# Performance work log

Measured on AMD Instinct MI355X. Metric: run time of the kernel, lower is better.

## Reference

```python
import jax, jax.numpy as jnp
import numpy as np
import math

B, S, H, NH = 8, 512, 1024, 16
DH = H // NH
MAX_REL = 64
LN_EPS = 1e-12


def _relpos_table(length, depth, max_rel=MAX_REL):
    # sinusoidal table over relative-distance vocab, gathered into [L, L, depth]
    vocab = 2 * max_rel + 1
    pos = np.arange(vocab, dtype=np.float32)[:, None]
    div = np.exp(np.arange(0, depth, 2, dtype=np.float32) * (-math.log(10000.0) / depth))
    table = np.zeros((vocab, depth), dtype=np.float32)
    table[:, 0::2] = np.sin(pos * div)
    table[:, 1::2] = np.cos(pos * div)
    r = np.arange(length)
    dist = np.clip(r[None, :] - r[:, None], -max_rel, max_rel) + max_rel  # [L,L], entry (i,j)=j-i
    return jnp.asarray(table[dist])  # [L, L, depth]


def _linear(x, W, b):  # torch layout: W [out, in]
    return jnp.einsum('...i,oi->...o', x, W) + b


def _gather_shift(seq, shift, valid_len):
    # seq [B,S,H]; out[i, j] = seq[i, j+shift[i]] for j < valid_len[i], else 0
    pos = jnp.arange(S)
    idx = jnp.clip(pos[None, :] + shift[:, None], 0, S - 1)  # [B,S]
    g = jnp.take_along_axis(seq, idx[:, :, None], axis=1)
    mask = pos[None, :] < valid_len[:, None]
    return jnp.where(mask[:, :, None], g, jnp.zeros((), seq.dtype))


def _nezha_attention(hs, enc, R, Wq, bq, Wk, bk, Wv, bv):
    def heads(x):  # [B,S,H] -> [B,NH,S,DH]
        return x.reshape(B, S, NH, DH).transpose(0, 2, 1, 3)
    q = heads(_linear(hs, Wq, bq))
    k = heads(_linear(enc, Wk, bk))
    v = heads(_linear(enc, Wv, bv))
    scores = jnp.einsum('bhqd,bhkd->bhqk', q, k)
    scores = scores + jnp.einsum('bhqd,qkd->bhqk', q, R)  # relative-key bias
    scores = scores / math.sqrt(DH)
    probs = jax.nn.softmax(scores, axis=-1)  # dropout: eval mode (identity)
    ctx = jnp.einsum('bhqk,bhkd->bhqd', probs, v)
    ctx = ctx + jnp.einsum('bhqk,qkd->bhqd', probs, R)  # relative-value term
    return ctx.transpose(0, 2, 1, 3).reshape(B, S, H)


def setup_inputs() -> dict:
    key = jax.random.key(0)
    ks = jax.random.split(key, 16)
    w = lambda k, shp: jax.random.normal(k, shp, jnp.float32) * 0.02
    return {
        'sequence_output': jax.random.normal(ks[0], (B, S, H), jnp.float32),
        'doc_len': jax.random.randint(ks[1], (B,), 0, 300, jnp.int32),
        'ques_len': jax.random.randint(ks[2], (B,), 0, 100, jnp.int32),
        'option_len': jax.random.randint(ks[3], (B,), 0, 100, jnp.int32),
        'Wq': w(ks[4], (H, H)), 'bq': jnp.zeros((H,), jnp.float32),
        'Wk': w(ks[5], (H, H)), 'bk': jnp.zeros((H,), jnp.float32),
        'Wv': w(ks[6], (H, H)), 'bv': jnp.zeros((H,), jnp.float32),
        'Wp': w(ks[7], (H, H)), 'bp': jnp.zeros((H,), jnp.float32),
        'Wo': w(ks[8], (H, H)), 'bo': jnp.zeros((H,), jnp.float32),
        'ln_g': jnp.ones((H,), jnp.float32), 'ln_b': jnp.zeros((H,), jnp.float32),
    }


def reference(sequence_output, doc_len, ques_len, option_len,
              Wq, bq, Wk, bk, Wv, bv, Wp, bp, Wo, bo, ln_g, ln_b):
    one = jnp.ones_like(doc_len)
    # seperate_seq (only the two tensors DUMA consumes)
    doc_seq = _gather_shift(sequence_output, one, doc_len)
    ques_opt = _gather_shift(sequence_output, doc_len + 1, ques_len + option_len)

    R = _relpos_table(S, DH)
    doc_enc = _nezha_attention(doc_seq, ques_opt, R, Wq, bq, Wk, bk, Wv, bv)
    qo_enc = _nezha_attention(ques_opt, doc_seq, R, Wq, bq, Wk, bk, Wv, bv)

    pooler = lambda x: jnp.tanh(_linear(x, Wp, bp))
    doc_pooled = pooler(doc_enc)
    qo_pooled = pooler(qo_enc)

    # BertSelfOutput: dense + (dropout=eval) + LayerNorm(residual)
    y = _linear(doc_pooled, Wo, bo) + qo_pooled
    mu = jnp.mean(y, axis=-1, keepdims=True)
    var = jnp.mean(jnp.square(y - mu), axis=-1, keepdims=True)
    y = (y - mu) * jax.lax.rsqrt(var + LN_EPS) * ln_g + ln_b

    return pooler(y)
```

## Files before the change

### kernel.cpp

```cpp
#include <hip/hip_runtime.h>
#include <hip/hip_bf16.h>
#include <cstdint>
#include <cstddef>

using bf16 = __hip_bfloat16;
typedef __attribute__((ext_vector_type(8))) short short8;
typedef __attribute__((ext_vector_type(4))) short short4v;
typedef __attribute__((ext_vector_type(4))) float f32x4;

#define KQLD 2048
#define SCL   0.18033688f
#define EXP2F(x) __builtin_amdgcn_exp2f(x)

__device__ __forceinline__ void gl2lds16(const bf16* g, void* l) {
  __builtin_amdgcn_global_load_lds((const __attribute__((address_space(1))) void*)g,
                                   (__attribute__((address_space(3))) void*)l, 16, 0, 0);
}

template<int ACT, bool OUTBF, bool HASB, int VTM>
__global__ __launch_bounds__(512)
void gemm_big(const bf16* __restrict__ A, const bf16* __restrict__ Bm,
              void* __restrict__ Cv, const float* __restrict__ bias,
              int N, int K, int lda, int ldb, int ldc, bf16* __restrict__ Vt)
{
  __shared__ __align__(16) short lA[3 * 4096];
  __shared__ __align__(16) short lB[3 * 8192];
  const int tid = threadIdx.x;
  int bx = blockIdx.x, by = blockIdx.y;
  {
    const int nwg = gridDim.x * gridDim.y;
    if ((nwg & 7) == 0) {
      int n = by * gridDim.x + bx;
      n = (n & 7) * (nwg >> 3) + (n >> 3);
      bx = n / gridDim.y;
      by = n % gridDim.y;
    }
  }
  const int m0 = bx * 128;
  const int n0 = by * 256;
  const int w = tid >> 6, lane = tid & 63;
  const int wr = (w >> 2) * 64, wc = (w & 3) * 64;
  const int lr = lane & 15, lg = lane >> 4;
  f32x4 acc[4][4] = {};
  const int ra = tid >> 2;
  const int xc = ((tid & 3) ^ ((tid >> 2) & 3)) * 8;
  const int e1 = tid + 512;
  const int rb1 = e1 >> 2;
  const bf16* pa0 = A + (long)(m0 + ra) * lda + xc;
  const bf16* pb0 = Bm + (long)(n0 + ra) * ldb + xc;
  const bf16* pb1 = Bm + (long)(n0 + rb1) * ldb + xc;

  #define GSTG(k0_, ofa_, ofb_) do {                  \
    gl2lds16(pa0 + (k0_), &lA[(ofa_) + tid * 8]);     \
    gl2lds16(pb0 + (k0_), &lB[(ofb_) + tid * 8]);     \
    gl2lds16(pb1 + (k0_), &lB[(ofb_) + e1 * 8]);      \
  } while (0)

  const int nT = K >> 5;
  GSTG(0, 0, 0);
  if (nT > 1) GSTG(32, 4096, 8192);
  if (nT > 2) asm volatile("s_waitcnt vmcnt(3)" ::: "memory");
  else        asm volatile("s_waitcnt vmcnt(0)" ::: "memory");
  __builtin_amdgcn_s_barrier();
  __builtin_amdgcn_sched_barrier(0);

  const int lgx = (lg ^ (lr & 3)) * 8;
  int oa = 0, oa1 = 4096, oa2 = 8192;
  int ob = 0, ob1 = 8192, ob2 = 16384;
  for (int t = 0; t < nT; ++t) {
    if (t + 2 < nT) GSTG((t + 2) * 32, oa2, ob2);
    short8 af[4], bfr[4];
    #pragma unroll
    for (int i = 0; i < 4; ++i) {
      af[i]  = *(const short8*)(&lA[oa + (wr + i * 16 + lr) * 32 + lgx]);
      bfr[i] = *(const short8*)(&lB[ob + (wc + i * 16 + lr) * 32 + lgx]);
    }
    #pragma unroll
    for (int mf = 0; mf < 4; ++mf)
      #pragma unroll
      for (int nf = 0; nf < 4; ++nf)
        acc[mf][nf] = __builtin_amdgcn_mfma_f32_16x16x32_bf16(af[mf], bfr[nf], acc[mf][nf], 0, 0, 0);
    if (t + 1 < nT) {
      if (t + 2 < nT) asm volatile("s_waitcnt vmcnt(3)" ::: "memory");
      else            asm volatile("s_waitcnt vmcnt(0)" ::: "memory");
      __builtin_amdgcn_s_barrier();
      __builtin_amdgcn_sched_barrier(0);
      int tmp = oa; oa = oa1; oa1 = oa2; oa2 = tmp;
      tmp = ob; ob = ob1; ob1 = ob2; ob2 = tmp;
    }
  }
  #undef GSTG

  #pragma unroll
  for (int nf = 0; nf < 4; ++nf) {
    const int col = n0 + wc + nf * 16 + lr;
    if (col >= N) continue;
    const float bv = HASB ? bias[col] : 0.0f;
    if (VTM && col >= 2048) {
      const int hd = col - 2048;
      const int d = hd & 63, hh = hd >> 6;
      #pragma unroll
      for (int mf = 0; mf < 4; ++mf) {
        const int row0 = m0 + wr + mf * 16 + lg * 4;
        const int zz = ((1 - (row0 >> 12)) << 7) | (((row0 >> 9) & 7) << 4) | hh;
        short4v pk;
        #pragma unroll
        for (int j = 0; j < 4; ++j)
          pk[j] = (short)__builtin_bit_cast(unsigned short,
                    __float2bfloat16(acc[mf][nf][j] + bv));
        *(short4v*)(Vt + ((long)(zz * 64 + d)) * 512 + (row0 & 511)) = pk;
      }
    } else {
      #pragma unroll
      for (int mf = 0; mf < 4; ++mf) {
        #pragma unroll
        for (int j = 0; j < 4; ++j) {
          const int row = m0 + wr + mf * 16 + lg * 4 + j;
          float x = acc[mf][nf][j] + bv;
          if (ACT == 1) x = tanhf(x);
          const long off = (long)row * ldc + col;
          if (OUTBF) ((bf16*)Cv)[off] = __float2bfloat16(x);
          else       ((float*)Cv)[off] = x;
        }
      }
    }
  }
}

template<int ACT, bool OUTBF, bool HASB>
__global__ __launch_bounds__(256)
void gemm_sm(const bf16* __restrict__ A, const bf16* __restrict__ Bm,
             void* __restrict__ Cv, const float* __restrict__ bias,
             int N, int K, int lda, int ldb, int ldc)
{
  __shared__ __align__(16) short lA[3 * 4096];
  __shared__ __align__(16) short lB[3 * 4096];
  const int tid = threadIdx.x;
  int bx = blockIdx.x, by = blockIdx.y;
  {
    const int nwg = gridDim.x * gridDim.y;
    if ((nwg & 7) == 0) {
      int n = by * gridDim.x + bx;
      n = (n & 7) * (nwg >> 3) + (n >> 3);
      bx = n / gridDim.y;
      by = n % gridDim.y;
    }
  }
  const int m0 = bx * 128;
  const int n0 = by * 128;
  const int w = tid >> 6, lane = tid & 63;
  const int wr = (w >> 1) * 64, wc = (w & 1) * 64;
  const int lr = lane & 15, lg = lane >> 4;
  f32x4 acc[4][4] = {};
  const int e0 = tid, e1 = tid + 256;
  const int r0_ = e0 >> 2;
  const int r1_ = e1 >> 2;
  const int xc = ((tid & 3) ^ ((tid >> 2) & 3)) * 8;
  const bf16* pa0 = A + (long)(m0 + r0_) * lda + xc;
  const bf16* pa1 = A + (long)(m0 + r1_) * lda + xc;
  const bf16* pb0 = Bm + (long)(n0 + r0_) * ldb + xc;
  const bf16* pb1 = Bm + (long)(n0 + r1_) * ldb + xc;

  #define GSTG2(k0_, off_) do {                       \
    gl2lds16(pa0 + (k0_), &lA[(off_) + e0 * 8]);      \
    gl2lds16(pa1 + (k0_), &lA[(off_) + e1 * 8]);      \
    gl2lds16(pb0 + (k0_), &lB[(off_) + e0 * 8]);      \
    gl2lds16(pb1 + (k0_), &lB[(off_) + e1 * 8]);      \
  } while (0)

  const int nT = K >> 5;
  GSTG2(0, 0);
  if (nT > 1) GSTG2(32, 4096);
  if (nT > 2) asm volatile("s_waitcnt vmcnt(4)" ::: "memory");
  else        asm volatile("s_waitcnt vmcnt(0)" ::: "memory");
  __builtin_amdgcn_s_barrier();
  __builtin_amdgcn_sched_barrier(0);

  const int lgx = (lg ^ (lr & 3)) * 8;
  int ofc = 0, of1 = 4096, of2 = 8192;
  for (int t = 0; t < nT; ++t) {
    if (t + 2 < nT) GSTG2((t + 2) * 32, of2);
    short8 af[4], bfr[4];
    #pragma unroll
    for (int i = 0; i < 4; ++i) {
      af[i]  = *(const short8*)(&lA[ofc + (wr + i * 16 + lr) * 32 + lgx]);
      bfr[i] = *(const short8*)(&lB[ofc + (wc + i * 16 + lr) * 32 + lgx]);
    }
    #pragma unroll
    for (int mf = 0; mf < 4; ++mf)
      #pragma unroll
      for (int nf = 0; nf < 4; ++nf)
        acc[mf][nf] = __builtin_amdgcn_mfma_f32_16x16x32_bf16(af[mf], bfr[nf], acc[mf][nf], 0, 0, 0);
    if (t + 1 < nT) {
      if (t + 2 < nT) asm volatile("s_waitcnt vmcnt(4)" ::: "memory");
      else            asm volatile("s_waitcnt vmcnt(0)" ::: "memory");
      __builtin_amdgcn_s_barrier();
      __builtin_amdgcn_sched_barrier(0);
      const int tmp = ofc; ofc = of1; of1 = of2; of2 = tmp;
    }
  }
  #undef GSTG2

  #pragma unroll
  for (int nf = 0; nf < 4; ++nf) {
    const int col = n0 + wc + nf * 16 + lr;
    if (col >= N) continue;
    const float bv = HASB ? bias[col] : 0.0f;
    #pragma unroll
    for (int mf = 0; mf < 4; ++mf) {
      #pragma unroll
      for (int j = 0; j < 4; ++j) {
        const int row = m0 + wr + mf * 16 + lg * 4 + j;
        float x = acc[mf][nf][j] + bv;
        if (ACT == 1) x = tanhf(x);
        const long off = (long)row * ldc + col;
        if (OUTBF) ((bf16*)Cv)[off] = __float2bfloat16(x);
        else       ((float*)Cv)[off] = x;
      }
    }
  }
}

__global__ __launch_bounds__(256)
void k_prep(const float* __restrict__ w0, const float* __restrict__ w1,
            const float* __restrict__ w2, const float* __restrict__ w3,
            const float* __restrict__ w4, bf16* __restrict__ wdst,
            const float* __restrict__ seq, const int* __restrict__ dl,
            const int* __restrict__ ql, const int* __restrict__ ol,
            bf16* __restrict__ X, bf16* __restrict__ tbl, bf16* __restrict__ tbt,
            const float* __restrict__ bq, const float* __restrict__ bk,
            const float* __restrict__ bv, float* __restrict__ biasq)
{
  const int bid = blockIdx.x, tid = threadIdx.x;
  if (bid < 5120) {
    const int bsel = bid >> 10;
    const float* s = bsel == 0 ? w0 : bsel == 1 ? w1 : bsel == 2 ? w2 : bsel == 3 ? w3 : w4;
    const float sc = (bsel == 0) ? SCL : 1.0f;
    const long loc = ((long)(bid & 1023) * 256 + tid) * 4;
    float4 v = *(const float4*)(s + loc);
    short4v pk;
    pk[0] = (short)__builtin_bit_cast(unsigned short, __float2bfloat16(v.x * sc));
    pk[1] = (short)__builtin_bit_cast(unsigned short, __float2bfloat16(v.y * sc));
    pk[2] = (short)__builtin_bit_cast(unsigned short, __float2bfloat16(v.z * sc));
    pk[3] = (short)__builtin_bit_cast(unsigned short, __float2bfloat16(v.w * sc));
    *(short4v*)(wdst + (long)bsel * 1048576 + loc) = pk;
  } else if (bid < 13312) {
    const int row = bid - 5120;
    const int c = tid * 4;
    const int b = (row >> 9) & 7, j = row & 511;
    int vlen, src;
    if (row < 4096) { vlen = dl[b]; src = (j + 1 > 511) ? 511 : j + 1; }
    else {
      vlen = ql[b] + ol[b];
      int s2 = j + dl[b] + 1;
      src = s2 > 511 ? 511 : (s2 < 0 ? 0 : s2);
    }
    float4 v = make_float4(0, 0, 0, 0);
    if (j < vlen) v = *(const float4*)(seq + ((long)b * 512 + src) * 1024 + c);
    short4v pk;
    pk[0] = (short)__builtin_bit_cast(unsigned short, __float2bfloat16(v.x));
    pk[1] = (short)__builtin_bit_cast(unsigned short, __float2bfloat16(v.y));
    pk[2] = (short)__builtin_bit_cast(unsigned short, __float2bfloat16(v.z));
    pk[3] = (short)__builtin_bit_cast(unsigned short, __float2bfloat16(v.w));
    *(short4v*)(X + (long)row * 1024 + c) = pk;
  } else {
    for (int idx = tid; idx < 144 * 64; idx += 256) {
      const int r = idx >> 6, d = idx & 63;
      float v = 0.0f;
      if (r < 129) {
        const float dv = powf(10000.0f, -(float)(d >> 1) / 32.0f);
        const float a = (float)r * dv;
        v = (d & 1) ? cosf(a) : sinf(a);
      }
      tbl[idx] = __float2bfloat16(v);
    }
    for (int idx = tid; idx < 64 * 160; idx += 256) {
      const int d = idx / 160, rr = idx % 160;
      float v = 0.0f;
      if (rr < 129) {
        const float dv = powf(10000.0f, -(float)(d >> 1) / 32.0f);
        const float a = (float)rr * dv;
        v = (d & 1) ? cosf(a) : sinf(a);
      }
      tbt[idx] = __float2bfloat16(v);
    }
    for (int idx = tid; idx < 3072; idx += 256) {
      float v = (idx < 1024) ? bq[idx] * SCL : (idx < 2048) ? bk[idx - 1024] : bv[idx - 2048];
      biasq[idx] = v;
    }
  }
}

__global__ __launch_bounds__(1024, 4)
void k_attn(const bf16* __restrict__ QKV, const bf16* __restrict__ Vt,
            const bf16* __restrict__ tbl, const bf16* __restrict__ tbt,
            bf16* __restrict__ ctx)
{
  __shared__ __align__(16) unsigned short s_kv[16384];
  __shared__ __align__(16) unsigned short s_ptile[16][16 * 72];
  __shared__ __align__(16) unsigned short s_m[16][16 * 132];

  const int tid = threadIdx.x;
  const int wv = tid >> 6, lane = tid & 63;
  const int lr = lane & 15, lg = lane >> 4;
  const int bid = blockIdx.x;
  const int xcd = bid & 7;
  const int idx = bid >> 3;
  const int z = (xcd << 5) | (idx >> 1);
  const int g = idx & 1;
  const int attn = z >> 7, b = (z >> 4) & 7, h = z & 15;
  const int qtok0 = attn * 4096 + b * 512;
  const int ktok0 = (1 - attn) * 4096 + b * 512;
  const int q0 = g * 256 + wv * 16;
  const int q = q0 + lr;

  unsigned short* ptile = s_ptile[wv];
  unsigned short* mrow  = s_m[wv];

  const bf16* Kbase = QKV + (long)ktok0 * KQLD + 1024 + h * 64;
  const bf16* Vbase = Vt + (long)z * (64 * 512);

  const int sl = tid & 511;
  const int rs = sl >> 3, cs = (sl & 7) * 8;
  const int scz = cs ^ ((rs & 7) << 3);
  const bool isV = tid >= 512;

  short8 qf[2];
  #pragma unroll
  for (int hh = 0; hh < 2; ++hh)
    qf[hh] = *(const short8*)(QKV + (long)(qtok0 + q0 + lr) * KQLD + h * 64 + hh * 32 + lg * 8);

  #define STAGE(kvb_, koff_, voff_) do {                                            \
    if (!isV) gl2lds16(Kbase + (long)((kvb_) + rs) * KQLD + scz, &s_kv[(koff_) + sl * 8]); \
    else      gl2lds16(Vbase + (long)rs * 512 + (kvb_) + scz,    &s_kv[(voff_) + sl * 8]); \
  } while (0)

  STAGE(0, 0, 8192);

  #pragma unroll
  for (int rt = 0; rt < 9; ++rt) {
    f32x4 qa = {};
    #pragma unroll
    for (int hh = 0; hh < 2; ++hh) {
      short8 ta = *(const short8*)(tbl + (rt * 16 + lr) * 64 + hh * 32 + lg * 8);
      qa = __builtin_amdgcn_mfma_f32_16x16x32_bf16(ta, qf[hh], qa, 0, 0, 0);
    }
    if (rt < 8 || lg == 0) {
      short4v pk;
      #pragma unroll
      for (int j = 0; j < 4; ++j)
        pk[j] = (short)__builtin_bit_cast(unsigned short, __float2bfloat16(qa[j]));
      *(short4v*)(&mrow[lr * 132 + rt * 16 + lg * 4]) = pk;
    }
  }

  const int hx = (lr >> 2) & 1;
  const int lgx8 = (lg ^ (lr & 3)) * 8;
  const int lrx64 = lr * 64;

  const float bias_lo = __bfloat162float(((const bf16*)mrow)[lr * 132 + 0]);
  const float bias_hi = __bfloat162float(((const bf16*)mrow)[lr * 132 + 128]);

  float l_run = 0.f, b0 = 0.f, b1 = 0.f;
  f32x4 cacc[4] = {};

  __syncthreads();

  #pragma unroll 2
  for (int t = 0; t < 8; ++t) {
    const int kvb = t * 64;
    const int koff = (t & 1) * 4096;
    const int voff = 8192 + koff;
    if (t < 7) { const int nk = ((t + 1) & 1) * 4096; STAGE(kvb + 64, nk, 8192 + nk); }

    f32x4 sc[4] = {};
    __builtin_amdgcn_s_setprio(1);
    #pragma unroll
    for (int hh = 0; hh < 2; ++hh) {
      const int cb = ((hh ^ hx) << 5) + lgx8;
      #pragma unroll
      for (int kb4 = 0; kb4 < 4; ++kb4) {
        short8 ak = *(const short8*)(&s_kv[koff + kb4 * 1024 + lrx64 + cb]);
        sc[kb4] = __builtin_amdgcn_mfma_f32_16x16x32_bf16(ak, qf[hh], sc[kb4], 0, 0, 0);
      }
    }
    __builtin_amdgcn_s_setprio(0);

    const int cls = (kvb + 63 <= q0 - 64) ? 0 : ((kvb >= q0 + 79) ? 2 : 1);

    float pacc[4];
    if (cls == 1) {
      const bool eLo = (kvb <= q0 - 49);
      const bool eHi = (kvb + 63 >= q0 + 64);
      short4v pks[4];
      #pragma unroll
      for (int kb4 = 0; kb4 < 4; ++kb4) {
        short4v pk;
        float ps = 0.f;
        #pragma unroll
        for (int j = 0; j < 4; ++j) {
          int rel = kvb + kb4 * 16 + 4 * lg + j - q;
          int rc = rel < -64 ? -64 : (rel > 64 ? 64 : rel);
          float bias = __bfloat162float(((const bf16*)mrow)[lr * 132 + rc + 64]);
          float p = EXP2F(sc[kb4][j] + bias);
          ps += p;
          if (eLo && rel <= -64) b0 += p;
          if (eHi && rel >= 64)  b1 += p;
          pk[j] = (short)__builtin_bit_cast(unsigned short, __float2bfloat16(p));
        }
        pks[kb4] = pk;
        pacc[kb4] = ps;
        *(short4v*)(&ptile[lr * 72 + kb4 * 16 + 4 * lg]) = pk;
      }
      l_run += (pacc[0] + pacc[1]) + (pacc[2] + pacc[3]);
      #pragma unroll
      for (int kb4 = 0; kb4 < 4; ++kb4)
        #pragma unroll
        for (int j = 0; j < 4; ++j) {
          int rel = kvb + kb4 * 16 + 4 * lg + j - q;
          if (rel > -64 && rel < 64)
            mrow[lr * 132 + rel + 63] = (unsigned short)pks[kb4][j];
        }
    } else {
      const float bc = (cls == 0) ? bias_lo : bias_hi;
      #pragma unroll
      for (int kb4 = 0; kb4 < 4; ++kb4) {
        short4v pk;
        float ps = 0.f;
        #pragma unroll
        for (int j = 0; j < 4; ++j) {
          float p = EXP2F(sc[kb4][j] + bc);
          ps += p;
          pk[j] = (short)__builtin_bit_cast(unsigned short, __float2bfloat16(p));
        }
        pacc[kb4] = ps;
        *(short4v*)(&ptile[lr * 72 + kb4 * 16 + 4 * lg]) = pk;
      }
      const float ts = (pacc[0] + pacc[1]) + (pacc[2] + pacc[3]);
      l_run += ts;
      if (cls == 0) b0 += ts; else b1 += ts;
    }

    __builtin_amdgcn_s_setprio(1);
    #pragma unroll
    for (int c2 = 0; c2 < 2; ++c2) {
      short8 pa = *(const short8*)(&ptile[lr * 72 + c2 * 32 + lg * 8]);
      const int cb = ((c2 ^ hx) << 5) + lgx8;
      #pragma unroll
      for (int nf = 0; nf < 4; ++nf) {
        short8 vb = *(const short8*)(&s_kv[voff + nf * 1024 + lrx64 + cb]);
        cacc[nf] = __builtin_amdgcn_mfma_f32_16x16x32_bf16(pa, vb, cacc[nf], 0, 0, 0);
      }
    }
    __builtin_amdgcn_s_setprio(0);
    __syncthreads();
  }
  #undef STAGE

  l_run += __shfl_xor(l_run, 16); l_run += __shfl_xor(l_run, 32);
  b0 += __shfl_xor(b0, 16); b0 += __shfl_xor(b0, 32);
  b1 += __shfl_xor(b1, 16); b1 += __shfl_xor(b1, 32);
  const float inv = 1.0f / l_run;

  #pragma unroll
  for (int j = 0; j < 4; ++j) {
    float iq = __shfl(inv, 4 * lg + j);
    #pragma unroll
    for (int nf = 0; nf < 4; ++nf) cacc[nf][j] *= iq;
  }
  short8 paf[5];
  #pragma unroll
  for (int c = 0; c < 5; ++c)
    #pragma unroll
    for (int j = 0; j < 8; ++j) {
      int r = c * 32 + 8 * lg + j;
      float v = 0.f;
      if (r == 0) v = b0;
      else if (r == 128) v = b1;
      else if (r < 128) {
        int k = q + r - 64;
        if (k >= 0 && k < 512)
          v = __bfloat162float(((const bf16*)mrow)[lr * 132 + r - 1]);
      }
      bf16 vb = __float2bfloat16(v * inv);
      paf[c][j] = (short)__builtin_bit_cast(unsigned short, vb);
    }
  __builtin_amdgcn_s_setprio(1);
  #pragma unroll
  for (int c = 0; c < 5; ++c)
    #pragma unroll
    for (int nf = 0; nf < 4; ++nf) {
      short8 tb = *(const short8*)(tbt + (nf * 16 + lr) * 160 + c * 32 + lg * 8);
      cacc[nf] = __builtin_amdgcn_mfma_f32_16x16x32_bf16(paf[c], tb, cacc[nf], 0, 0, 0);
    }
  __builtin_amdgcn_s_setprio(0);
  #pragma unroll
  for (int nf = 0; nf < 4; ++nf)
    #pragma unroll
    for (int j = 0; j < 4; ++j) {
      int qq = q0 + 4 * lg + j;
      ctx[(long)(qtok0 + qq) * 1024 + h * 64 + nf * 16 + lr] = __float2bfloat16(cacc[nf][j]);
    }
}

__global__ __launch_bounds__(256) void k_ln(const float* __restrict__ y,
    const bf16* __restrict__ pooled, const float* __restrict__ g,
    const float* __restrict__ be, bf16* __restrict__ o)
{
  const int row = blockIdx.x, tid = threadIdx.x;
  float x[4], s1 = 0.0f, s2 = 0.0f;
  #pragma unroll
  for (int i = 0; i < 4; ++i) {
    const int c = tid + i * 256;
    x[i] = y[(long)row * 1024 + c] + __bfloat162float(pooled[(long)(4096 + row) * 1024 + c]);
    s1 += x[i]; s2 += x[i] * x[i];
  }
  #pragma unroll
  for (int off = 1; off < 64; off <<= 1) { s1 += __shfl_xor(s1, off); s2 += __shfl_xor(s2, off); }
  __shared__ float r1[4], r2[4];
  if ((tid & 63) == 0) { r1[tid >> 6] = s1; r2[tid >> 6] = s2; }
  __syncthreads();
  s1 = r1[0] + r1[1] + r1[2] + r1[3];
  s2 = r2[0] + r2[1] + r2[2] + r2[3];
  const float mu = s1 * (1.0f / 1024.0f);
  const float var = s2 * (1.0f / 1024.0f) - mu * mu;
  const float rs = rsqrtf(var + 1e-12f);
  #pragma unroll
  for (int i = 0; i < 4; ++i) {
    const int c = tid + i * 256;
    o[(long)row * 1024 + c] = __float2bfloat16((x[i] - mu) * rs * g[c] + be[c]);
  }
}

__global__ void k_sent(float* o, float v) { o[0] = v; }

extern "C" void kernel_launch(void* const* d_in, const int* in_sizes, int n_in,
                              void* d_out, int out_size, void* d_ws, size_t ws_size,
                              hipStream_t stream)
{
  (void)in_sizes; (void)n_in; (void)out_size;
  const float* seq = (const float*)d_in[0];
  const int*  dl = (const int*)d_in[1];
  const int*  ql = (const int*)d_in[2];
  const int*  ol = (const int*)d_in[3];
  const float* Wq = (const float*)d_in[4];  const float* bq = (const float*)d_in[5];
  const float* Wk = (const float*)d_in[6];  const float* bk = (const float*)d_in[7];
  const float* Wv = (const float*)d_in[8];  const float* bv = (const float*)d_in[9];
  const float* Wp = (const float*)d_in[10]; const float* bp = (const float*)d_in[11];
  const float* Wo = (const float*)d_in[12]; const float* bo = (const float*)d_in[13];
  const float* lng = (const float*)d_in[14]; const float* lnb = (const float*)d_in[15];
  float* out = (float*)d_out;
  char* ws = (char*)d_ws;

  size_t cur = 0;
  auto alloc = [&](size_t bts) { size_t o = cur; cur += (bts + 255) & ~(size_t)255; return o; };
  const size_t oBIAS = alloc(3072 * sizeof(float));
  const size_t oTBL  = alloc(144 * 64 * 2);
  const size_t oTBT  = alloc(64 * 160 * 2);
  const size_t oWBF  = alloc(5ull * 1048576 * 2);
  const size_t oXBF  = alloc(8192ull * 1024 * 2);
  const size_t oQKV  = alloc(8192ull * KQLD * 2);
  const size_t oQR   = alloc(8192ull * 2176 * 2);
  const size_t oBP   = alloc(256ull * 64 * 512 * 2);
  if (ws_size < cur) {
    k_sent<<<1, 1, 0, stream>>>(out, 1.0e6f + (float)(ws_size >> 20));
    return;
  }

  float* biasq = (float*)(ws + oBIAS);
  bf16* tbl = (bf16*)(ws + oTBL);
  bf16* tbt = (bf16*)(ws + oTBT);
  bf16* wqb = (bf16*)(ws + oWBF);
  bf16* wpb = wqb + 3 * 1048576;
  bf16* wob = wqb + 4 * 1048576;
  bf16* xbf = (bf16*)(ws + oXBF);
  bf16* qkv = (bf16*)(ws + oQKV);
  bf16* bpb = (bf16*)(ws + oBP);
  bf16* ctx = xbf;
  bf16* pooled = (bf16*)(ws + oQR);
  float* ybuf = (float*)(ws + oQR + 8192ull * 1024 * 2);
  bf16* yln = (bf16*)(ws + oBP);

  dim3 blk(256);
  k_prep<<<13313, blk, 0, stream>>>(Wq, Wk, Wv, Wp, Wo, wqb,
                                    seq, dl, ql, ol, xbf, tbl, tbt,
                                    bq, bk, bv, biasq);

  gemm_big<0, true, true, 1><<<dim3(64, 12, 1), dim3(512), 0, stream>>>(xbf, wqb, qkv, biasq, 3072, 1024, 1024, 1024, KQLD, bpb);
  k_attn<<<512, dim3(1024), 0, stream>>>(qkv, bpb, tbl, tbt, ctx);

  gemm_big<1, true, true, 0><<<dim3(64, 4, 1), dim3(512), 0, stream>>>(ctx, wpb, pooled, bp, 1024, 1024, 1024, 1024, 1024, nullptr);
  gemm_sm<0, false, true><<<dim3(32, 8, 1), blk, 0, stream>>>(pooled, wob, ybuf, bo, 1024, 1024, 1024, 1024, 1024);
  k_ln<<<4096, blk, 0, stream>>>(ybuf, pooled, lng, lnb, yln);
  gemm_sm<1, false, true><<<dim3(32, 8, 1), blk, 0, stream>>>(yln, wpb, out, bp, 1024, 1024, 1024, 1024, 1024);
}
```

Before: 283.9 us.

## Replace QKV projection GEMM with 256x256-tile ping-pong pipelined kernel

Adds a new gemm8p kernel that computes the fused Q/K/V projection with 256x256 output tiles and a K-step of 64. It double-buffers four LDS sub-tiles, interleaves the global-to-LDS loads for the next step between MFMA phases, and raises wave priority around the MFMA bursts. The goal is to overlap memory loads with matrix-core work and get more reuse per tile than the previous gemm_big launch. In exchange it halves the number of workgroups in the grid (32x12 instead of 64x12), uses 128 KB of LDS, and hardcodes K=1024 with hand-tuned waitcnt values.

```diff
diff --git a/kernel.cpp b/kernel.cpp
--- a/kernel.cpp
+++ b/kernel.cpp
@@ -15,6 +15,122 @@
 __device__ __forceinline__ void gl2lds16(const bf16* g, void* l) {
   __builtin_amdgcn_global_load_lds((const __attribute__((address_space(1))) void*)g,
                                    (__attribute__((address_space(3))) void*)l, 16, 0, 0);
+}
+
+template<int VTM>
+__global__ __launch_bounds__(512, 2)
+void gemm8p(const bf16* __restrict__ A, const bf16* __restrict__ Bm,
+            bf16* __restrict__ C, const float* __restrict__ bias,
+            int lda, int ldb, int ldc, bf16* __restrict__ Vt)
+{
+  __shared__ __align__(16) short lds[2 * 4 * 8192];
+  const int tid = threadIdx.x;
+  int bx = blockIdx.x, by = blockIdx.y;
+  {
+    const int nwg = gridDim.x * gridDim.y;
+    int n = by * gridDim.x + bx;
+    n = (n & 7) * (nwg >> 3) + (n >> 3);
+    bx = n / gridDim.y;
+    by = n % gridDim.y;
+  }
+  const int m0 = bx * 256, n0 = by * 256;
+  const int w = tid >> 6, lane = tid & 63;
+  const int wm = w >> 2, wn = w & 3;
+  const int lr = lane & 15, lg = lane >> 4;
+
+  const bf16* pa = A + (long)(m0 + (tid >> 2)) * lda + (tid & 3) * 8;
+  const bf16* pb = Bm + (long)(n0 + (tid >> 2)) * ldb + (tid & 3) * 8;
+  const long ldaL = (long)lda * 128, ldbL = (long)ldb * 128;
+
+  #define STG(Q_, kt_) do {                                          \
+    const int sq_ = (((kt_) & 1) * 4 + (Q_)) * 8192;                 \
+    const int k0_ = (kt_) * 64 + ((Q_) >> 1) * 32;                   \
+    const bf16* s_ = (((Q_) & 1) ? pb : pa) + k0_;                   \
+    const long l_ = ((Q_) & 1) ? ldbL : ldaL;                        \
+    gl2lds16(s_,      &lds[sq_ + tid * 8]);                          \
+    gl2lds16(s_ + l_, &lds[sq_ + (tid + 512) * 8]);                  \
+  } while (0)
+
+  f32x4 ac[2][4][4] = {};
+
+  STG(0, 0); STG(1, 0); STG(2, 0); STG(3, 0); STG(0, 1);
+  asm volatile("s_waitcnt vmcnt(6)" ::: "memory");
+  __builtin_amdgcn_s_barrier();
+  __builtin_amdgcn_sched_barrier(0);
+
+  short8 bfv[4];
+  for (int t = 0; t < 16; ++t) {
+    const int s = (t & 1) * 4;
+    #pragma unroll
+    for (int p = 0; p < 4; ++p) {
+      const int mh = p & 1, ks = p >> 1;
+      short8 af[4];
+      #pragma unroll
+      for (int i = 0; i < 4; ++i)
+        af[i] = *(const short8*)(&lds[(s + ks * 2) * 8192 +
+                 (wm * 128 + mh * 64 + i * 16 + lr) * 32 + lg * 8]);
+      if (mh == 0) {
+        #pragma unroll
+        for (int j = 0; j < 4; ++j)
+          bfv[j] = *(const short8*)(&lds[(s + ks * 2 + 1) * 8192 +
+                   (wn * 64 + j * 16 + lr) * 32 + lg * 8]);
+      }
+      if (p == 0 && t < 15) STG(1, t + 1);
+      if (p == 1 && t < 15) STG(2, t + 1);
+      if (p == 2 && t < 15) STG(3, t + 1);
+      if (p == 3 && t < 14) STG(0, t + 2);
+      __builtin_amdgcn_s_barrier();
+      asm volatile("s_waitcnt lgkmcnt(0)" ::: "memory");
+      __builtin_amdgcn_sched_barrier(0);
+      __builtin_amdgcn_s_setprio(1);
+      #pragma unroll
+      for (int i = 0; i < 4; ++i)
+        #pragma unroll
+        for (int j = 0; j < 4; ++j)
+          ac[mh][i][j] = __builtin_amdgcn_mfma_f32_16x16x32_bf16(af[i], bfv[j], ac[mh][i][j], 0, 0, 0);
+      __builtin_amdgcn_s_setprio(0);
+      if (p == 1) {
+        if (t < 15) asm volatile("s_waitcnt vmcnt(6)" ::: "memory");
+        else        asm volatile("s_waitcnt vmcnt(0)" ::: "memory");
+      } else if (p == 3) {
+        if (t < 14)       asm volatile("s_waitcnt vmcnt(6)" ::: "memory");
+        else if (t == 14) asm volatile("s_waitcnt vmcnt(4)" ::: "memory");
+      }
+      if (!(t == 15 && p == 3)) __builtin_amdgcn_s_barrier();
+      __builtin_amdgcn_sched_barrier(0);
+    }
+  }
+  #undef STG
+
+  #pragma unroll
+  for (int mh = 0; mh < 2; ++mh)
+    #pragma unroll
+    for (int nf = 0; nf < 4; ++nf) {
+      const int col = n0 + wn * 64 + nf * 16 + lr;
+      const float bv = bias[col];
+      if (VTM && col >= 2048) {
+        const int hd = col - 2048, d = hd & 63, hh = hd >> 6;
+        #pragma unroll
+        for (int i = 0; i < 4; ++i) {
+          const int row0 = m0 + wm * 128 + mh * 64 + i * 16 + lg * 4;
+          const int zz = ((1 - (row0 >> 12)) << 7) | (((row0 >> 9) & 7) << 4) | hh;
+          short4v pk;
+          #pragma unroll
+          for (int j = 0; j < 4; ++j)
+            pk[j] = (short)__builtin_bit_cast(unsigned short,
+                      __float2bfloat16(ac[mh][i][nf][j] + bv));
+          *(short4v*)(Vt + ((long)(zz * 64 + d)) * 512 + (row0 & 511)) = pk;
+        }
+      } else {
+        #pragma unroll
+        for (int i = 0; i < 4; ++i)
+          #pragma unroll
+          for (int j = 0; j < 4; ++j) {
+            const int row = m0 + wm * 128 + mh * 64 + i * 16 + lg * 4 + j;
+            C[(long)row * ldc + col] = __float2bfloat16(ac[mh][i][nf][j] + bv);
+          }
+      }
+    }
 }
 
 template<int ACT, bool OUTBF, bool HASB, int VTM>
@@ -586,7 +702,7 @@
                                     seq, dl, ql, ol, xbf, tbl, tbt,
                                     bq, bk, bv, biasq);
 
-  gemm_big<0, true, true, 1><<<dim3(64, 12, 1), dim3(512), 0, stream>>>(xbf, wqb, qkv, biasq, 3072, 1024, 1024, 1024, KQLD, bpb);
+  gemm8p<1><<<dim3(32, 12), dim3(512), 0, stream>>>(xbf, wqb, qkv, biasq, 1024, 1024, KQLD, bpb);
   k_attn<<<512, dim3(1024), 0, stream>>>(qkv, bpb, tbl, tbt, ctx);
 
   gemm_big<1, true, true, 0><<<dim3(64, 4, 1), dim3(512), 0, stream>>>(ctx, wpb, pooled, bp, 1024, 1024, 1024, 1024, 1024, nullptr);
```

Result: no change. 286.5 us (+0.9%).
